# Kernel tuning notes

Hardware: AMD Instinct MI355X
Metric: run time of the kernel (lower is better)

Reference implementation:

```python
import jax, jax.numpy as jnp
import numpy as np

OFFSET = 3  # (kernel_size - 1) // 2 with kernel_size = 7
NEG_INF = -1e30


def conv1x1(x, W, b):
    # x: (B, Cin, H, W), W: (Cout, Cin), b: (Cout,)
    return jnp.einsum('oi,bihw->bohw', W, x) + b[None, :, None, None]


def local_attention(Q, K, V, offset):
    """Per-pixel windowed cross-attention, vectorized over all pixels.

    Faithful to LocalAttentionLayer: for each (h, w) the query attends over
    K/V entries with indices in [max(0, h-off), min(S-1, h+off)] x [...],
    softmax over the (variable-size) window, output = attn-weighted sum of V.
    Q, K: (B, Ch, H, W); V: (B, C, H, W) -> out (B, C, H, W).
    """
    B, Ch, H, W = Q.shape
    k = 2 * offset + 1
    pad = ((0, 0), (0, 0), (offset, offset), (offset, offset))
    Kp = jnp.pad(K, pad)
    Vp = jnp.pad(V, pad)
    valid = jnp.pad(jnp.ones((H, W), dtype=bool),
                    ((offset, offset), (offset, offset)))

    scores = []  # k*k entries of (B, H, W)
    masks = []
    for dh in range(k):
        for dw in range(k):
            Ks = Kp[:, :, dh:dh + H, dw:dw + W]
            scores.append(jnp.einsum('bchw,bchw->bhw', Q, Ks))
            masks.append(valid[dh:dh + H, dw:dw + W])
    scores = jnp.stack(scores, axis=-1)          # (B, H, W, k*k)
    mask = jnp.stack(masks, axis=-1)             # (H, W, k*k)
    scores = jnp.where(mask[None], scores, NEG_INF)
    attn = jax.nn.softmax(scores, axis=-1)       # window softmax per pixel

    out = jnp.zeros_like(V)
    i = 0
    for dh in range(k):
        for dw in range(k):
            Vs = Vp[:, :, dh:dh + H, dw:dw + W]  # (B, C, H, W)
            out = out + attn[:, None, :, :, i] * Vs
            i += 1
    return out


def reference(left_features, right_features, Wq, bq, Wk, bk,
              vis_CA, self_attend, same_WqWk):
    def attend(query_features, key_features):
        Q = conv1x1(query_features, Wq, bq)
        if same_WqWk:
            K = conv1x1(key_features, Wq, bq)
        else:
            K = conv1x1(key_features, Wk, bk)
        return local_attention(Q, K, key_features, OFFSET)

    weighted_r = attend(left_features, right_features)
    if self_attend:
        weighted_l = attend(left_features, left_features)
        return jnp.concatenate([weighted_l, weighted_r], axis=1)
    return jnp.concatenate([left_features, weighted_r], axis=1)


def setup_inputs() -> dict:
    key = jax.random.key(0)
    ks = jax.random.split(key, 6)
    B, Cin, Ch, H, W = 256, 128, 64, 32, 32
    return {
        'left_features': jax.random.normal(ks[0], (B, Cin, H, W), jnp.float32),
        'right_features': jax.random.normal(ks[1], (B, Cin, H, W), jnp.float32),
        'Wq': jax.random.normal(ks[2], (Ch, Cin), jnp.float32) * (1.0 / np.sqrt(Cin)),
        'bq': jax.random.normal(ks[3], (Ch,), jnp.float32) * 0.01,
        'Wk': jax.random.normal(ks[4], (Ch, Cin), jnp.float32) * (1.0 / np.sqrt(Cin)),
        'bk': jax.random.normal(ks[5], (Ch,), jnp.float32) * 0.01,
        'vis_CA': 0,
        'self_attend': 1,
        'same_WqWk': 0,
    }
```

## Files before the change

### kernel.cpp

```cpp
#include <hip/hip_runtime.h>
#include <hip/hip_fp16.h>

#define B_    256
#define CIN   128
#define CH    64
#define NPX   1024
#define NWIN  49
#define TROWS 22
#define TCOLS 40
#define CELLU 4
#define BUFU  (TROWS * TCOLS * CELLU)
#define NEG_INF_F (-1e30f)

typedef _Float16 h2v __attribute__((ext_vector_type(2)));
typedef __fp16   p2v __attribute__((ext_vector_type(2)));

#define FDOT2(a, b, c) __builtin_amdgcn_fdot2((a), (b), (c), false)

union CV { p2v p; h2v h; uint u; };
union U4 { int4 v; uint u[4]; h2v h[4]; };

#define FMIX(acc, vu, vh, pu, ph) do {                                                                              \
    if      ((vh) == 0 && (ph) == 0) asm("v_fma_mix_f32 %0, %1, %2, %0 op_sel:[0,0,0] op_sel_hi:[1,1,0]" : "+v"(acc) : "v"(vu), "v"(pu)); \
    else if ((vh) == 1 && (ph) == 0) asm("v_fma_mix_f32 %0, %1, %2, %0 op_sel:[1,0,0] op_sel_hi:[1,1,0]" : "+v"(acc) : "v"(vu), "v"(pu)); \
    else if ((vh) == 0 && (ph) == 1) asm("v_fma_mix_f32 %0, %1, %2, %0 op_sel:[0,1,0] op_sel_hi:[1,1,0]" : "+v"(acc) : "v"(vu), "v"(pu)); \
    else                             asm("v_fma_mix_f32 %0, %1, %2, %0 op_sel:[1,1,0] op_sel_hi:[1,1,0]" : "+v"(acc) : "v"(vu), "v"(pu)); \
} while (0)

#define PKFMA(accu, vu, pu, ph) do {                                                                                \
    if ((ph) == 0) asm("v_pk_fma_f16 %0, %2, %1, %0 op_sel:[0,0,0] op_sel_hi:[0,1,1]" : "+v"(accu) : "v"(vu), "v"(pu)); \
    else           asm("v_pk_fma_f16 %0, %2, %1, %0 op_sel:[1,0,0] op_sel_hi:[1,1,1]" : "+v"(accu) : "v"(vu), "v"(pu)); \
} while (0)

#define FLUSHLO(a32, pk) asm("v_fma_mix_f32 %0, 1.0, %1, %0 op_sel:[0,0,0] op_sel_hi:[0,1,0]" : "+v"(a32) : "v"(pk))
#define FLUSHHI(a32, pk) asm("v_fma_mix_f32 %0, 1.0, %1, %0 op_sel:[0,1,0] op_sel_hi:[0,1,0]" : "+v"(a32) : "v"(pk))

__global__ __launch_bounds__(256) void wtrans_kernel(
    const float* __restrict__ Wq, const float* __restrict__ Wk,
    const int* __restrict__ same_flag,
    uint* __restrict__ WtPQ, uint* __restrict__ WtPK)
{
    const float* Wsel = (same_flag[0] != 0) ? Wq : Wk;
    for (int idx = threadIdx.x; idx < (CIN / 2) * CH; idx += 256) {
        int i2 = idx >> 6;
        int o  = idx & 63;
        CV a; a.p = __builtin_amdgcn_cvt_pkrtz(Wq[o * CIN + 2 * i2], Wq[o * CIN + 2 * i2 + 1]);
        WtPQ[idx] = a.u;
        CV b2; b2.p = __builtin_amdgcn_cvt_pkrtz(Wsel[o * CIN + 2 * i2], Wsel[o * CIN + 2 * i2 + 1]);
        WtPK[idx] = b2.u;
    }
}

__global__ __launch_bounds__(256, 4) void conv3_kernel(
    const float* __restrict__ left, const float* __restrict__ right,
    const uint* __restrict__ WtPQ, const uint* __restrict__ WtPK,
    const float* __restrict__ bq, const float* __restrict__ bk,
    const int* __restrict__ same_flag,
    uint* __restrict__ dQ, uint* __restrict__ dKL, uint* __restrict__ dKR)
{
    int which = blockIdx.y;
    const float* x    = (which == 2) ? right : left;
    const uint*  Wt   = (which == 0) ? WtPQ : WtPK;
    const float* bias = (which == 0 || same_flag[0] != 0) ? bq : bk;
    uint* dst         = (which == 0) ? dQ : ((which == 1) ? dKL : dKR);

    int b  = blockIdx.x >> 2;
    int px = ((blockIdx.x & 3) << 8) + threadIdx.x;
    const float* xb = x + (size_t)b * (CIN * NPX) + px;

    float acc[CH];
#pragma unroll
    for (int o = 0; o < CH; ++o) acc[o] = bias[o];

#pragma unroll 8
    for (int i2 = 0; i2 < CIN / 2; ++i2) {
        float x0 = xb[(size_t)(2 * i2) << 10];
        float x1 = xb[(size_t)(2 * i2 + 1) << 10];
        CV xp; xp.p = __builtin_amdgcn_cvt_pkrtz(x0, x1);
        const uint* wrow = Wt + (i2 << 6);
#pragma unroll
        for (int o = 0; o < CH; ++o) {
            CV wv; wv.u = wrow[o];
            acc[o] = FDOT2(xp.h, wv.h, acc[o]);
        }
    }

    uint* db = dst + (size_t)b * ((CH / 2) * NPX) + px;
#pragma unroll
    for (int o2 = 0; o2 < CH / 2; ++o2) {
        CV cv; cv.p = __builtin_amdgcn_cvt_pkrtz(acc[2 * o2], acc[2 * o2 + 1]);
        db[(size_t)o2 << 10] = cv.u;
    }
}

__global__ __launch_bounds__(256) __attribute__((amdgpu_waves_per_eu(2, 2)))
void attend2_kernel(
    const uint* __restrict__ Q, const uint* __restrict__ KR,
    const uint* __restrict__ KL,
    const float* __restrict__ right, const float* __restrict__ left,
    float* __restrict__ out, const int* __restrict__ self_flag)
{
    __shared__ __align__(16) uint buf[2 * BUFU];

    int side = blockIdx.y;
    int b    = blockIdx.x >> 1;
    int h0   = (blockIdx.x & 1) << 4;
    int t    = threadIdx.x;
    int w    = t & 31;
    int r2   = (t >> 5) << 1;
    int h    = h0 + r2;
    int qoff = (h << 5) + w;
    int cb   = side ? 0 : CIN;

    const uint*  K = side ? KL : KR;
    const float* V = side ? left : right;

    if (side == 1 && self_flag[0] == 0) {
        const float* s = left + (size_t)b * (CIN * NPX) + qoff;
        float* d = out + (size_t)b * (2 * CIN * NPX) + qoff;
        for (int c = 0; c < CIN; ++c) {
            d[(size_t)c << 10] = s[(size_t)c << 10];
            d[((size_t)c << 10) + 32] = s[((size_t)c << 10) + 32];
        }
        return;
    }

#pragma unroll
    for (int i = 0; i < 7; ++i) {
        int idx = t + (i << 8);
        if (idx < 2 * BUFU / 4) ((int4*)buf)[idx] = int4{0, 0, 0, 0};
    }

    int rowlo = (h0 == 0) ? 0 : h0 - 3;
    int rowof = (h0 == 0) ? 3 : 0;
    int c2    = (t >> 5) & 3;
    int rr    = t >> 7;

    const uint* Kb = K + (size_t)b * ((CH / 2) * NPX);
    const uint* Qb = Q + (size_t)b * ((CH / 2) * NPX);

    float sc0[NWIN], sc1[NWIN];
#pragma unroll
    for (int i = 0; i < NWIN; ++i) { sc0[i] = 0.f; sc1[i] = 0.f; }

#define ROWS_OK(i) (rr + 2 * (i) < 19)
#define PFK(g, arr)                                                            \
    _Pragma("unroll") for (int i = 0; i < 10; ++i) if (ROWS_OK(i))             \
        arr[i] = Kb[((size_t)((((g) << 2) + c2)) << 10) + ((rowlo + rr + 2 * i) << 5) + w];
#define WRK(bp, arr)                                                           \
    _Pragma("unroll") for (int i = 0; i < 10; ++i) if (ROWS_OK(i))             \
        (bp)[((rowof + rr + 2 * i) * TCOLS + (w + 4)) * CELLU + c2] = arr[i];

#define COMPA(bp, g) {                                                         \
    CV qa[4], qc[4];                                                           \
    _Pragma("unroll") for (int j = 0; j < 4; ++j) {                            \
        qa[j].u = Qb[((size_t)(((g) << 2) + j) << 10) + qoff];                 \
        qc[j].u = Qb[((size_t)(((g) << 2) + j) << 10) + qoff + 32];            \
    }                                                                          \
    _Pragma("unroll") for (int dh = 0; dh < 8; ++dh) {                         \
        int cu0 = ((r2 + dh) * TCOLS + (w + 1)) * CELLU;                       \
        _Pragma("unroll") for (int dw = 0; dw < 7; ++dw) {                     \
            U4 kk; kk.v = *(const int4*)((bp) + cu0 + dw * CELLU);             \
            if (dh < 7) {                                                      \
                float s = sc0[dh * 7 + dw];                                    \
                _Pragma("unroll") for (int j = 0; j < 4; ++j)                  \
                    s = FDOT2(kk.h[j], qa[j].h, s);                            \
                sc0[dh * 7 + dw] = s;                                          \
            }                                                                  \
            if (dh >= 1) {                                                     \
                float s = sc1[(dh - 1) * 7 + dw];                              \
                _Pragma("unroll") for (int j = 0; j < 4; ++j)                  \
                    s = FDOT2(kk.h[j], qc[j].h, s);                            \
                sc1[(dh - 1) * 7 + dw] = s;                                    \
            }                                                                  \
        }                                                                      \
    } }

    {
        uint pfa[10], pfb[10];
        PFK(0, pfa); PFK(1, pfb);
#pragma unroll 1
        for (int gp = 0; gp < 4; ++gp) {
            __syncthreads();
            WRK(buf, pfa); WRK(buf + BUFU, pfb);
            if (gp < 3) { PFK(2 * gp + 2, pfa); PFK(2 * gp + 3, pfb); }
            __syncthreads();
            COMPA(buf, 2 * gp);
            COMPA(buf + BUFU, 2 * gp + 1);
        }
    }

    uint ph0[25], ph1[25];
    {
        float m = NEG_INF_F;
#pragma unroll
        for (int dh = 0; dh < 7; ++dh)
#pragma unroll
            for (int dw = 0; dw < 7; ++dw) {
                int i = dh * 7 + dw;
                bool vld = ((unsigned)(h + dh - 3) < 32u) && ((unsigned)(w + dw - 3) < 32u);
                sc0[i] = vld ? sc0[i] : NEG_INF_F;
                m = fmaxf(m, sc0[i]);
            }
        float ssum = 0.f;
#pragma unroll
        for (int i = 0; i < NWIN; ++i) { sc0[i] = __expf(sc0[i] - m); ssum += sc0[i]; }
        float inv = 1.f / ssum;
#pragma unroll
        for (int j = 0; j < 24; ++j) {
            CV cv; cv.p = __builtin_amdgcn_cvt_pkrtz(sc0[2 * j] * inv, sc0[2 * j + 1] * inv);
            ph0[j] = cv.u;
        }
        CV cv; cv.p = __builtin_amdgcn_cvt_pkrtz(sc0[48] * inv, 0.f);
        ph0[24] = cv.u;
    }
    {
        float m = NEG_INF_F;
#pragma unroll
        for (int dh = 0; dh < 7; ++dh)
#pragma unroll
            for (int dw = 0; dw < 7; ++dw) {
                int i = dh * 7 + dw;
                bool vld = ((unsigned)(h + 1 + dh - 3) < 32u) && ((unsigned)(w + dw - 3) < 32u);
                sc1[i] = vld ? sc1[i] : NEG_INF_F;
                m = fmaxf(m, sc1[i]);
            }
        float ssum = 0.f;
#pragma unroll
        for (int i = 0; i < NWIN; ++i) { sc1[i] = __expf(sc1[i] - m); ssum += sc1[i]; }
        float inv = 1.f / ssum;
#pragma unroll
        for (int j = 0; j < 24; ++j) {
            CV cv; cv.p = __builtin_amdgcn_cvt_pkrtz(sc1[2 * j] * inv, sc1[2 * j + 1] * inv);
            ph1[j] = cv.u;
        }
        CV cv; cv.p = __builtin_amdgcn_cvt_pkrtz(sc1[48] * inv, 0.f);
        ph1[24] = cv.u;
    }

    const float* Vb = V + (size_t)b * (CIN * NPX);
    float* ob = out + (size_t)b * (2 * CIN * NPX) + ((size_t)cb << 10) + qoff;

    float pv0[10], pv1[10];
#define PFV(vg) {                                                              \
    const float* va = Vb + ((size_t)((((vg) << 2) + c2) * 2) << 10);           \
    const float* vc = va + NPX;                                                \
    _Pragma("unroll") for (int i = 0; i < 10; ++i) if (ROWS_OK(i)) {           \
        int gi = ((rowlo + rr + 2 * i) << 5) + w;                              \
        pv0[i] = va[gi]; pv1[i] = vc[gi];                                      \
    } }
#define WRV(bp)                                                                \
    _Pragma("unroll") for (int i = 0; i < 10; ++i) if (ROWS_OK(i)) {           \
        CV cv; cv.p = __builtin_amdgcn_cvt_pkrtz(pv0[i], pv1[i]);              \
        (bp)[((rowof + rr + 2 * i) * TCOLS + (w + 4)) * CELLU + c2] = cv.u;    \
    }

    PFV(0);
    __syncthreads();
    WRV(buf);

#pragma unroll 1
    for (int vg = 0; vg < 16; ++vg) {
        if (vg < 15) PFV(vg + 1);
        __syncthreads();

        const uint* bp = buf + (vg & 1) * BUFU;
        float a0[8], a1[8];
#pragma unroll
        for (int c = 0; c < 8; ++c) { a0[c] = 0.f; a1[c] = 0.f; }
        uint pk0[4], pk1[4];
#pragma unroll
        for (int j = 0; j < 4; ++j) { pk0[j] = 0u; pk1[j] = 0u; }

#pragma unroll
        for (int dh = 0; dh < 8; ++dh) {
            int cu0 = ((r2 + dh) * TCOLS + (w + 1)) * CELLU;
#pragma unroll
            for (int dw = 0; dw < 7; ++dw) {
                U4 kk; kk.v = *(const int4*)(bp + cu0 + dw * CELLU);
                if (dh < 7) {
                    int tp = dh * 7 + dw;
#pragma unroll
                    for (int j = 0; j < 4; ++j)
                        PKFMA(pk0[j], kk.u[j], ph0[tp >> 1], (tp & 1));
                }
                if (dh >= 1) {
                    int tp = (dh - 1) * 7 + dw;
#pragma unroll
                    for (int j = 0; j < 4; ++j)
                        PKFMA(pk1[j], kk.u[j], ph1[tp >> 1], (tp & 1));
                }
            }
            if (dh & 1) {
#pragma unroll
                for (int j = 0; j < 4; ++j) {
                    FLUSHLO(a0[2 * j], pk0[j]); FLUSHHI(a0[2 * j + 1], pk0[j]); pk0[j] = 0u;
                    FLUSHLO(a1[2 * j], pk1[j]); FLUSHHI(a1[2 * j + 1], pk1[j]); pk1[j] = 0u;
                }
            }
        }

        if (vg < 15) WRV(buf + ((vg + 1) & 1) * BUFU);

#pragma unroll
        for (int c = 0; c < 8; ++c) {
            ob[((size_t)((vg << 3) + c)) << 10] = a0[c];
            ob[(((size_t)((vg << 3) + c)) << 10) + 32] = a1[c];
        }
    }
}

extern "C" void kernel_launch(void* const* d_in, const int* in_sizes, int n_in,
                              void* d_out, int out_size, void* d_ws, size_t ws_size,
                              hipStream_t stream)
{
    (void)in_sizes; (void)n_in; (void)out_size; (void)ws_size;

    const float* left  = (const float*)d_in[0];
    const float* right = (const float*)d_in[1];
    const float* Wq    = (const float*)d_in[2];
    const float* bq    = (const float*)d_in[3];
    const float* Wk    = (const float*)d_in[4];
    const float* bk    = (const float*)d_in[5];
    const int* self_flag = (const int*)d_in[7];
    const int* same_flag = (const int*)d_in[8];

    uint* wsQ  = (uint*)d_ws;
    uint* wsKL = wsQ  + (size_t)B_ * (CH / 2) * NPX;
    uint* wsKR = wsKL + (size_t)B_ * (CH / 2) * NPX;
    uint* WtPQ = wsKR + (size_t)B_ * (CH / 2) * NPX;
    uint* WtPK = WtPQ + (CIN / 2) * CH;

    float* out = (float*)d_out;

    wtrans_kernel<<<1, 256, 0, stream>>>(Wq, Wk, same_flag, WtPQ, WtPK);

    conv3_kernel<<<dim3(B_ * 4, 3), 256, 0, stream>>>(
        left, right, WtPQ, WtPK, bq, bk, same_flag, wsQ, wsKL, wsKR);

    attend2_kernel<<<dim3(B_ * 2, 2), 256, 0, stream>>>(
        wsQ, wsKR, wsKL, right, left, out, self_flag);
}
```

Before: 298.8 us.

## Compute 1x1 projections with MFMA and share left input between Q and K

Replaces the scalar fdot2 1x1 conv kernel with an MFMA 16x16x32 f16 GEMM. Weights are pre-swizzled into the A-fragment layout and each wave loads a B fragment of 16 pixels by 128 channels. The left image is now read once for both the Q and K_left projections instead of in separate blocks, cutting input traffic by a third. The conv was taking a notable share of the time next to the attention kernel, and this frees VALU work for matrix cores. In exchange, global loads per lane are strided by channel, which may lower coalescing efficiency.

```diff
diff --git a/kernel.cpp b/kernel.cpp
--- a/kernel.cpp
+++ b/kernel.cpp
@@ -14,11 +14,14 @@
 
 typedef _Float16 h2v __attribute__((ext_vector_type(2)));
 typedef __fp16   p2v __attribute__((ext_vector_type(2)));
+typedef __fp16   p8v __attribute__((ext_vector_type(8)));
+typedef float    f4v __attribute__((ext_vector_type(4)));
 
 #define FDOT2(a, b, c) __builtin_amdgcn_fdot2((a), (b), (c), false)
 
 union CV { p2v p; h2v h; uint u; };
 union U4 { int4 v; uint u[4]; h2v h[4]; };
+union AF { uint4 u4; p8v h8; };
 
 #define FMIX(acc, vu, vh, pu, ph) do {                                                                              \
     if      ((vh) == 0 && (ph) == 0) asm("v_fma_mix_f32 %0, %1, %2, %0 op_sel:[0,0,0] op_sel_hi:[1,1,0]" : "+v"(acc) : "v"(vu), "v"(pu)); \
@@ -38,59 +41,81 @@
 __global__ __launch_bounds__(256) void wtrans_kernel(
     const float* __restrict__ Wq, const float* __restrict__ Wk,
     const int* __restrict__ same_flag,
-    uint* __restrict__ WtPQ, uint* __restrict__ WtPK)
+    uint* __restrict__ WAQ, uint* __restrict__ WAK)
 {
     const float* Wsel = (same_flag[0] != 0) ? Wq : Wk;
-    for (int idx = threadIdx.x; idx < (CIN / 2) * CH; idx += 256) {
-        int i2 = idx >> 6;
-        int o  = idx & 63;
-        CV a; a.p = __builtin_amdgcn_cvt_pkrtz(Wq[o * CIN + 2 * i2], Wq[o * CIN + 2 * i2 + 1]);
-        WtPQ[idx] = a.u;
-        CV b2; b2.p = __builtin_amdgcn_cvt_pkrtz(Wsel[o * CIN + 2 * i2], Wsel[o * CIN + 2 * i2 + 1]);
-        WtPK[idx] = b2.u;
+    for (int idx = threadIdx.x; idx < 4096; idx += 256) {
+        int j  = idx & 3;
+        int l  = (idx >> 2) & 63;
+        int ks = (idx >> 8) & 3;
+        int mt = idx >> 10;
+        int row = mt * 16 + (l & 15);
+        int k0  = ks * 32 + ((l >> 4) << 3) + 2 * j;
+        CV a; a.p = __builtin_amdgcn_cvt_pkrtz(Wq[row * CIN + k0], Wq[row * CIN + k0 + 1]);
+        WAQ[idx] = a.u;
+        CV b2; b2.p = __builtin_amdgcn_cvt_pkrtz(Wsel[row * CIN + k0], Wsel[row * CIN + k0 + 1]);
+        WAK[idx] = b2.u;
     }
 }
 
-__global__ __launch_bounds__(256, 4) void conv3_kernel(
+__global__ __launch_bounds__(256) void convm_kernel(
     const float* __restrict__ left, const float* __restrict__ right,
-    const uint* __restrict__ WtPQ, const uint* __restrict__ WtPK,
+    const uint* __restrict__ WAQ, const uint* __restrict__ WAK,
     const float* __restrict__ bq, const float* __restrict__ bk,
     const int* __restrict__ same_flag,
     uint* __restrict__ dQ, uint* __restrict__ dKL, uint* __restrict__ dKR)
 {
-    int which = blockIdx.y;
-    const float* x    = (which == 2) ? right : left;
-    const uint*  Wt   = (which == 0) ? WtPQ : WtPK;
-    const float* bias = (which == 0 || same_flag[0] != 0) ? bq : bk;
-    uint* dst         = (which == 0) ? dQ : ((which == 1) ? dKL : dKR);
-
-    int b  = blockIdx.x >> 2;
-    int px = ((blockIdx.x & 3) << 8) + threadIdx.x;
-    const float* xb = x + (size_t)b * (CIN * NPX) + px;
-
-    float acc[CH];
-#pragma unroll
-    for (int o = 0; o < CH; ++o) acc[o] = bias[o];
-
-#pragma unroll 8
-    for (int i2 = 0; i2 < CIN / 2; ++i2) {
-        float x0 = xb[(size_t)(2 * i2) << 10];
-        float x1 = xb[(size_t)(2 * i2 + 1) << 10];
-        CV xp; xp.p = __builtin_amdgcn_cvt_pkrtz(x0, x1);
-        const uint* wrow = Wt + (i2 << 6);
-#pragma unroll
-        for (int o = 0; o < CH; ++o) {
-            CV wv; wv.u = wrow[o];
-            acc[o] = FDOT2(xp.h, wv.h, acc[o]);
-        }
-    }
-
-    uint* db = dst + (size_t)b * ((CH / 2) * NPX) + px;
-#pragma unroll
-    for (int o2 = 0; o2 < CH / 2; ++o2) {
-        CV cv; cv.p = __builtin_amdgcn_cvt_pkrtz(acc[2 * o2], acc[2 * o2 + 1]);
-        db[(size_t)o2 << 10] = cv.u;
-    }
+    int t   = threadIdx.x;
+    int l   = t & 63;
+    int wv  = t >> 6;
+    int img = blockIdx.x >> 4;
+    int px  = ((blockIdx.x & 15) << 6) + (wv << 4) + (l & 15);
+    int che = (l >> 4) << 3;
+    int r0  = (l >> 4) << 2;
+    const float* biasK = (same_flag[0] != 0) ? bq : bk;
+
+    const float* xb = ((blockIdx.y == 0) ? left : right) + (size_t)img * (CIN * NPX);
+
+    AF bf[4];
+#pragma unroll
+    for (int ks = 0; ks < 4; ++ks) {
+        uint bu[4];
+#pragma unroll
+        for (int j = 0; j < 4; ++j) {
+            int ch = ks * 32 + che + 2 * j;
+            float x0 = xb[((size_t)ch << 10) + px];
+            float x1 = xb[((size_t)(ch + 1) << 10) + px];
+            CV c; c.p = __builtin_amdgcn_cvt_pkrtz(x0, x1);
+            bu[j] = c.u;
+        }
+        bf[ks].u4 = make_uint4(bu[0], bu[1], bu[2], bu[3]);
+    }
+
+#define DOGEMM(WA, BIAS, DST)                                                   \
+    {                                                                           \
+      uint* dst = DST + (size_t)img * ((CH / 2) * NPX);                         \
+      _Pragma("unroll") for (int mt = 0; mt < 4; ++mt) {                        \
+        float4 bb = *(const float4*)((BIAS) + mt * 16 + r0);                    \
+        f4v acc = { bb.x, bb.y, bb.z, bb.w };                                   \
+        _Pragma("unroll") for (int ks = 0; ks < 4; ++ks) {                      \
+            AF wa; wa.u4 = *(const uint4*)((WA) + (((mt << 2) + ks) << 8) + (l << 2)); \
+            acc = __builtin_amdgcn_mfma_f32_16x16x32_f16(wa.h8, bf[ks].h8, acc, 0, 0, 0); \
+        }                                                                       \
+        int cp = (mt << 3) + ((l >> 4) << 1);                                   \
+        CV c0; c0.p = __builtin_amdgcn_cvt_pkrtz(acc[0], acc[1]);               \
+        dst[((size_t)cp << 10) + px] = c0.u;                                    \
+        CV c1; c1.p = __builtin_amdgcn_cvt_pkrtz(acc[2], acc[3]);               \
+        dst[((size_t)(cp + 1) << 10) + px] = c1.u;                              \
+      }                                                                         \
+    }
+
+    if (blockIdx.y == 0) {
+        DOGEMM(WAQ, bq,    dQ)
+        DOGEMM(WAK, biasK, dKL)
+    } else {
+        DOGEMM(WAK, biasK, dKR)
+    }
+#undef DOGEMM
 }
 
 __global__ __launch_bounds__(256) __attribute__((amdgpu_waves_per_eu(2, 2)))
@@ -328,15 +353,15 @@
     uint* wsQ  = (uint*)d_ws;
     uint* wsKL = wsQ  + (size_t)B_ * (CH / 2) * NPX;
     uint* wsKR = wsKL + (size_t)B_ * (CH / 2) * NPX;
-    uint* WtPQ = wsKR + (size_t)B_ * (CH / 2) * NPX;
-    uint* WtPK = WtPQ + (CIN / 2) * CH;
+    uint* WAQ  = wsKR + (size_t)B_ * (CH / 2) * NPX;
+    uint* WAK  = WAQ + 4096;
 
     float* out = (float*)d_out;
 
-    wtrans_kernel<<<1, 256, 0, stream>>>(Wq, Wk, same_flag, WtPQ, WtPK);
-
-    conv3_kernel<<<dim3(B_ * 4, 3), 256, 0, stream>>>(
-        left, right, WtPQ, WtPK, bq, bk, same_flag, wsQ, wsKL, wsKR);
+    wtrans_kernel<<<1, 256, 0, stream>>>(Wq, Wk, same_flag, WAQ, WAK);
+
+    convm_kernel<<<dim3(B_ * 16, 2), 256, 0, stream>>>(
+        left, right, WAQ, WAK, bq, bk, same_flag, wsQ, wsKL, wsKR);
 
     attend2_kernel<<<dim3(B_ * 2, 2), 256, 0, stream>>>(
         wsQ, wsKR, wsKL, right, left, out, self_flag);
```

Result: faster. 267.3 us (-10.5%).
